# Optimization experiments

Hardware: AMD Instinct MI355X
Metric: run time of the kernel (lower is better)

## Reference

```python
import jax, jax.numpy as jnp
import numpy as np

N, M, D = 16384, 1024, 32


def setup_inputs() -> dict:
    key = jax.random.key(0)
    k1, k2 = jax.random.split(key)
    x = jax.random.normal(k1, (N, D), dtype=jnp.float32)
    centers = jax.random.normal(k2, (M, D), dtype=jnp.float32)
    sigma = jnp.ones((M, D), dtype=jnp.float32)  # get_sigma_ones(s=1.0)
    return {"x": x, "centers": centers, "sigma": sigma}


def reference(x, centers, sigma):
    # Gaussian RBF kernel: exp(-0.5 * delta^T invCov delta) / sqrt((2pi)^D det(S))
    d = x.shape[1]
    s2 = sigma ** 2  # (M, D)
    # invCovMat: inverse of per-center diagonal covariance -> diag(1/s2)
    invCov = jnp.eye(d, dtype=x.dtype) * (1.0 / s2)[:, :, None]  # (M, D, D)
    # denom: sqrt((2pi)^D * prod(s2))
    k = (2.0 * np.pi) ** d  # python float, safe for D=32 in f32
    detS = jnp.sqrt(jnp.asarray(k, x.dtype) * jnp.prod(s2, axis=1))  # (M,)
    delta = x[:, None, :] - centers[None, :, :]  # (N, M, D)
    # batched (1,D) @ (D,D) per (n,m) pair, then elementwise * delta and reduce
    q = jnp.einsum('nmd,mde->nme', delta, invCov)  # (N, M, D)
    X = jnp.sum(q * delta, axis=2)  # (N, M) squared Mahalanobis distance
    return jnp.exp(-0.5 * X) / detS[None, :]  # (N, M)
```

## Files before the change

kernel.cpp:

```cpp
#include <hip/hip_runtime.h>


#define N_  16384
#define M_  1024
#define D_  32
#define NT  32
#define BLK 256

typedef float v2f __attribute__((ext_vector_type(2)));

__global__ __launch_bounds__(BLK) void rbf_kernel(
    const float* __restrict__ x, const float* __restrict__ centers,
    const float* __restrict__ sigma, float* __restrict__ out)
{
    const int tid = threadIdx.x;
    const int m   = blockIdx.x * BLK + tid;
    const int n0  = blockIdx.y * NT;

    __shared__ float r2s[NT];

    if (tid < NT) {
        const float4* xr = (const float4*)(x + (size_t)(n0 + tid) * D_);
        float a0 = 0.f, a1 = 0.f, a2 = 0.f, a3 = 0.f;
        #pragma unroll
        for (int k = 0; k < D_ / 4; ++k) {
            float4 v = xr[k];
            a0 = fmaf(v.x, v.x, a0); a1 = fmaf(v.y, v.y, a1);
            a2 = fmaf(v.z, v.z, a2); a3 = fmaf(v.w, v.w, a3);
        }
        r2s[tid] = (a0 + a1) + (a2 + a3);
    }
    __syncthreads();

    const float L2E      = 1.4426950408889634f;
    const float LOG2_2PI = 2.6514961294723187f;

    float s2_0 = 0.f, ld = 0.f;
    bool uf = true;
    {
        const float* sg = sigma + (size_t)m * D_;
        #pragma unroll
        for (int d = 0; d < D_; ++d) {
            float s  = sg[d];
            float s2 = s * s;
            if (d == 0) s2_0 = s2;
            uf = uf && (s2 == s2_0);
            ld += log2f(s2);
        }
    }

    if (__all((int)uf)) {
        const float w0 = 1.0f / s2_0;
        v2f av[D_ / 2];
        float b = 0.f;
        {
            const v2f* cg = (const v2f*)(centers + (size_t)m * D_);
            #pragma unroll
            for (int j = 0; j < D_ / 2; ++j) {
                v2f c = cg[j];
                v2f a = c * w0;
                av[j] = a;
                b = fmaf(c.x, a.x, b);
                b = fmaf(c.y, a.y, b);
            }
        }
        const float c0 = fmaf(-0.5f * L2E, b, -0.5f * (D_ * LOG2_2PI + ld));
        const float qc = -0.5f * L2E * w0;

        float* o0 = out + (size_t)n0 * M_ + m;
        #pragma unroll 1
        for (int i = 0; i < NT; i += 2) {
            const v2f* xr0 = (const v2f*)(x + (size_t)(n0 + i) * D_);
            const v2f* xr1 = xr0 + (D_ / 2);
            v2f p0 = {0.f,0.f}, p1 = {0.f,0.f};
            v2f q0 = {0.f,0.f}, q1 = {0.f,0.f};
            #pragma unroll
            for (int j = 0; j < D_ / 2; j += 2) {
                p0 += xr0[j]     * av[j];
                p1 += xr0[j + 1] * av[j + 1];
                q0 += xr1[j]     * av[j];
                q1 += xr1[j + 1] * av[j + 1];
            }
            v2f ps = p0 + p1;
            v2f qs = q0 + q1;
            float f0 = fmaf(L2E, ps.x + ps.y, fmaf(qc, r2s[i],     c0));
            float f1 = fmaf(L2E, qs.x + qs.y, fmaf(qc, r2s[i + 1], c0));
            __builtin_nontemporal_store(__builtin_amdgcn_exp2f(f0), o0 + (size_t)i * M_);
            __builtin_nontemporal_store(__builtin_amdgcn_exp2f(f1), o0 + (size_t)(i + 1) * M_);
        }
    } else {
        const float c0 = -0.5f * (D_ * LOG2_2PI + ld);
        const float* cg = centers + (size_t)m * D_;
        const float* sg = sigma   + (size_t)m * D_;
        #pragma unroll 1
        for (int i = 0; i < NT; ++i) {
            const float* xr = x + (size_t)(n0 + i) * D_;
            float a0 = 0.f, a1 = 0.f;
            #pragma unroll
            for (int d = 0; d < D_; d += 2) {
                float s0 = sg[d], s1 = sg[d + 1];
                float t0 = xr[d]     - cg[d];
                float t1 = xr[d + 1] - cg[d + 1];
                a0 = fmaf(t0 * (1.0f / (s0 * s0)), t0, a0);
                a1 = fmaf(t1 * (1.0f / (s1 * s1)), t1, a1);
            }
            float f = fmaf(-0.5f * L2E, a0 + a1, c0);
            out[(size_t)(n0 + i) * M_ + m] = __builtin_amdgcn_exp2f(f);
        }
    }
}

extern "C" void kernel_launch(void* const* d_in, const int* in_sizes, int n_in,
                              void* d_out, int out_size, void* d_ws, size_t ws_size,
                              hipStream_t stream) {
    const float* x = (const float*)d_in[0];
    const float* c = (const float*)d_in[1];
    const float* s = (const float*)d_in[2];
    float* out = (float*)d_out;
    dim3 grid(M_ / BLK, N_ / NT);
    rbf_kernel<<<grid, BLK, 0, stream>>>(x, c, s, out);
}
```

Measured before the change: 97.66 us.

## Stage x tile and center/sigma rows in LDS, two centers per thread

After: 94.66 us. -3.1%, faster.

```diff
diff --git a/kernel.cpp b/kernel.cpp
--- a/kernel.cpp
+++ b/kernel.cpp
@@ -1,111 +1,160 @@
 #include <hip/hip_runtime.h>
 
 
-#define N_  16384
-#define M_  1024
-#define D_  32
-#define NT  32
-#define BLK 256
+#define N_   16384
+#define M_   1024
+#define D_   32
+#define NT   64
+#define BLK  256
+#define MW   (BLK / 64)
+#define SSTR 33
 
-typedef float v2f __attribute__((ext_vector_type(2)));
+typedef float v4f __attribute__((ext_vector_type(4)));
 
-__global__ __launch_bounds__(BLK) void rbf_kernel(
+__global__ __launch_bounds__(BLK, 2) void rbf_kernel(
     const float* __restrict__ x, const float* __restrict__ centers,
     const float* __restrict__ sigma, float* __restrict__ out)
 {
-    const int tid = threadIdx.x;
-    const int m   = blockIdx.x * BLK + tid;
-    const int n0  = blockIdx.y * NT;
+    const int tid  = threadIdx.x;
+    const int lane = tid & 63;
+    const int wv   = tid >> 6;
+    const int n0   = blockIdx.y * NT;
+    const int mbA  = blockIdx.x * (BLK * 2) + wv * 64;
+    const int mbB  = mbA + BLK;
 
+    __shared__ float xs[NT * D_];
     __shared__ float r2s[NT];
+    __shared__ float scr[MW][64 * SSTR];
 
-    if (tid < NT) {
-        const float4* xr = (const float4*)(x + (size_t)(n0 + tid) * D_);
-        float a0 = 0.f, a1 = 0.f, a2 = 0.f, a3 = 0.f;
+    {
+        const float4* xg  = (const float4*)(x + (size_t)n0 * D_);
+        float4*       xs4 = (float4*)xs;
         #pragma unroll
-        for (int k = 0; k < D_ / 4; ++k) {
-            float4 v = xr[k];
-            a0 = fmaf(v.x, v.x, a0); a1 = fmaf(v.y, v.y, a1);
-            a2 = fmaf(v.z, v.z, a2); a3 = fmaf(v.w, v.w, a3);
+        for (int j = 0; j < (NT * D_ / 4) / BLK; ++j) {
+            int f = j * BLK + tid;
+            float4 v = xg[f];
+            xs4[f] = v;
+            float s = fmaf(v.x, v.x, fmaf(v.y, v.y, fmaf(v.z, v.z, v.w * v.w)));
+            s += __shfl_xor(s, 1);
+            s += __shfl_xor(s, 2);
+            s += __shfl_xor(s, 4);
+            if ((tid & 7) == 0) r2s[f >> 3] = s;
         }
-        r2s[tid] = (a0 + a1) + (a2 + a3);
     }
     __syncthreads();
+
+    float* sw = scr[wv];
+
+    auto stagechunk = [&](const float* P, int mbase) {
+        const float4* P4 = (const float4*)(P + (size_t)mbase * D_);
+        #pragma unroll
+        for (int k = 0; k < 8; ++k) {
+            int f = k * 64 + lane;
+            float4 v = P4[f];
+            int off = (f >> 3) * SSTR + (f & 7) * 4;
+            sw[off + 0] = v.x; sw[off + 1] = v.y;
+            sw[off + 2] = v.z; sw[off + 3] = v.w;
+        }
+    };
+
+    auto sigscan = [&](int mbase, float& s2_0, float& ld) -> bool {
+        stagechunk(sigma, mbase);
+        const float* row = sw + lane * SSTR;
+        float s0 = row[0];
+        s2_0 = s0 * s0;
+        bool uf = true; ld = 0.f;
+        #pragma unroll
+        for (int d = 0; d < D_; ++d) {
+            float s  = row[d];
+            float s2 = s * s;
+            uf = uf && (s2 == s2_0);
+            ld += log2f(s2);
+        }
+        return uf;
+    };
+
+    auto cscan = [&](int mbase, float w0, v4f* A) -> float {
+        stagechunk(centers, mbase);
+        const float* row = sw + lane * SSTR;
+        float b = 0.f;
+        #pragma unroll
+        for (int k = 0; k < 8; ++k) {
+            v4f c = { row[4*k], row[4*k+1], row[4*k+2], row[4*k+3] };
+            v4f a = c * w0;
+            A[k] = a;
+            b = fmaf(c.x, a.x, fmaf(c.y, a.y, fmaf(c.z, a.z, fmaf(c.w, a.w, b))));
+        }
+        return b;
+    };
+
+    float s2A, ldA, s2B, ldB;
+    v4f A0[8], A1[8];
+    bool ufA = sigscan(mbA, s2A, ldA);
+    const float w0A = 1.0f / s2A;
+    float bA = cscan(mbA, w0A, A0);
+    bool ufB = sigscan(mbB, s2B, ldB);
+    const float w0B = 1.0f / s2B;
+    float bB = cscan(mbB, w0B, A1);
 
     const float L2E      = 1.4426950408889634f;
     const float LOG2_2PI = 2.6514961294723187f;
 
-    float s2_0 = 0.f, ld = 0.f;
-    bool uf = true;
-    {
-        const float* sg = sigma + (size_t)m * D_;
+    if (__all((int)(ufA && ufB))) {
         #pragma unroll
-        for (int d = 0; d < D_; ++d) {
-            float s  = sg[d];
-            float s2 = s * s;
-            if (d == 0) s2_0 = s2;
-            uf = uf && (s2 == s2_0);
-            ld += log2f(s2);
+        for (int k = 0; k < 8; ++k) {
+            asm volatile("" : "+v"(A0[k]));
+            asm volatile("" : "+v"(A1[k]));
         }
-    }
+        const float c0A = fmaf(-0.5f * L2E, bA, -0.5f * (D_ * LOG2_2PI + ldA));
+        const float c0B = fmaf(-0.5f * L2E, bB, -0.5f * (D_ * LOG2_2PI + ldB));
+        const float qcA = -0.5f * L2E * w0A;
+        const float qcB = -0.5f * L2E * w0B;
 
-    if (__all((int)uf)) {
-        const float w0 = 1.0f / s2_0;
-        v2f av[D_ / 2];
-        float b = 0.f;
-        {
-            const v2f* cg = (const v2f*)(centers + (size_t)m * D_);
+        float* oA = out + (size_t)n0 * M_ + mbA + lane;
+        float* oB = oA + BLK;
+        #pragma unroll 1
+        for (int i = 0; i < NT; ++i) {
+            const v4f* xr = (const v4f*)(xs + i * D_);
+            v4f pa = {0,0,0,0}, pb = {0,0,0,0};
+            v4f qa = {0,0,0,0}, qb = {0,0,0,0};
             #pragma unroll
-            for (int j = 0; j < D_ / 2; ++j) {
-                v2f c = cg[j];
-                v2f a = c * w0;
-                av[j] = a;
-                b = fmaf(c.x, a.x, b);
-                b = fmaf(c.y, a.y, b);
+            for (int k = 0; k < 8; k += 2) {
+                v4f x0 = xr[k], x1 = xr[k + 1];
+                pa += x0 * A0[k];     pb += x1 * A0[k + 1];
+                qa += x0 * A1[k];     qb += x1 * A1[k + 1];
             }
-        }
-        const float c0 = fmaf(-0.5f * L2E, b, -0.5f * (D_ * LOG2_2PI + ld));
-        const float qc = -0.5f * L2E * w0;
-
-        float* o0 = out + (size_t)n0 * M_ + m;
-        #pragma unroll 1
-        for (int i = 0; i < NT; i += 2) {
-            const v2f* xr0 = (const v2f*)(x + (size_t)(n0 + i) * D_);
-            const v2f* xr1 = xr0 + (D_ / 2);
-            v2f p0 = {0.f,0.f}, p1 = {0.f,0.f};
-            v2f q0 = {0.f,0.f}, q1 = {0.f,0.f};
-            #pragma unroll
-            for (int j = 0; j < D_ / 2; j += 2) {
-                p0 += xr0[j]     * av[j];
-                p1 += xr0[j + 1] * av[j + 1];
-                q0 += xr1[j]     * av[j];
-                q1 += xr1[j + 1] * av[j + 1];
-            }
-            v2f ps = p0 + p1;
-            v2f qs = q0 + q1;
-            float f0 = fmaf(L2E, ps.x + ps.y, fmaf(qc, r2s[i],     c0));
-            float f1 = fmaf(L2E, qs.x + qs.y, fmaf(qc, r2s[i + 1], c0));
-            __builtin_nontemporal_store(__builtin_amdgcn_exp2f(f0), o0 + (size_t)i * M_);
-            __builtin_nontemporal_store(__builtin_amdgcn_exp2f(f1), o0 + (size_t)(i + 1) * M_);
+            v4f ps = pa + pb, qs = qa + qb;
+            float SA = (ps.x + ps.y) + (ps.z + ps.w);
+            float SB = (qs.x + qs.y) + (qs.z + qs.w);
+            float r2 = r2s[i];
+            float fA = fmaf(L2E, SA, fmaf(qcA, r2, c0A));
+            float fB = fmaf(L2E, SB, fmaf(qcB, r2, c0B));
+            __builtin_nontemporal_store(__builtin_amdgcn_exp2f(fA), oA + (size_t)i * M_);
+            __builtin_nontemporal_store(__builtin_amdgcn_exp2f(fB), oB + (size_t)i * M_);
         }
     } else {
-        const float c0 = -0.5f * (D_ * LOG2_2PI + ld);
-        const float* cg = centers + (size_t)m * D_;
-        const float* sg = sigma   + (size_t)m * D_;
         #pragma unroll 1
-        for (int i = 0; i < NT; ++i) {
-            const float* xr = x + (size_t)(n0 + i) * D_;
-            float a0 = 0.f, a1 = 0.f;
-            #pragma unroll
-            for (int d = 0; d < D_; d += 2) {
-                float s0 = sg[d], s1 = sg[d + 1];
-                float t0 = xr[d]     - cg[d];
-                float t1 = xr[d + 1] - cg[d + 1];
-                a0 = fmaf(t0 * (1.0f / (s0 * s0)), t0, a0);
-                a1 = fmaf(t1 * (1.0f / (s1 * s1)), t1, a1);
+        for (int half = 0; half < 2; ++half) {
+            const int m = (half ? mbB : mbA) + lane;
+            const float* cg = centers + (size_t)m * D_;
+            const float* sg = sigma   + (size_t)m * D_;
+            const float ld  = half ? ldB : ldA;
+            const float c0  = -0.5f * (D_ * LOG2_2PI + ld);
+            #pragma unroll 1
+            for (int i = 0; i < NT; ++i) {
+                const float* xr = xs + i * D_;
+                float a0 = 0.f, a1 = 0.f;
+                #pragma unroll
+                for (int d = 0; d < D_; d += 2) {
+                    float s0 = sg[d], s1 = sg[d + 1];
+                    float t0 = xr[d]     - cg[d];
+                    float t1 = xr[d + 1] - cg[d + 1];
+                    a0 = fmaf(t0 * (1.0f / (s0 * s0)), t0, a0);
+                    a1 = fmaf(t1 * (1.0f / (s1 * s1)), t1, a1);
+                }
+                float f = fmaf(-0.5f * L2E, a0 + a1, c0);
+                out[(size_t)(n0 + i) * M_ + m] = __builtin_amdgcn_exp2f(f);
             }
-            float f = fmaf(-0.5f * L2E, a0 + a1, c0);
-            out[(size_t)(n0 + i) * M_ + m] = __builtin_amdgcn_exp2f(f);
         }
     }
 }
@@ -117,6 +166,6 @@
     const float* c = (const float*)d_in[1];
     const float* s = (const float*)d_in[2];
     float* out = (float*)d_out;
-    dim3 grid(M_ / BLK, N_ / NT);
+    dim3 grid(M_ / (BLK * 2), N_ / NT);
     rbf_kernel<<<grid, BLK, 0, stream>>>(x, c, s, out);
 }
```

## Register-block four centers per thread and stage x tile in LDS

Applied to the files above, without the earlier changes.

After: 113.0 us. 15.7% more time.

```diff
diff --git a/kernel.cpp b/kernel.cpp
--- a/kernel.cpp
+++ b/kernel.cpp
@@ -1,111 +1,136 @@
 #include <hip/hip_runtime.h>
 
 
-#define N_  16384
-#define M_  1024
-#define D_  32
-#define NT  32
-#define BLK 256
+#define N_   16384
+#define M_   1024
+#define D_   32
+#define NT   16
+#define BLK  256
 
 typedef float v2f __attribute__((ext_vector_type(2)));
+typedef float v4f __attribute__((ext_vector_type(4)));
 
-__global__ __launch_bounds__(BLK) void rbf_kernel(
+__global__ __launch_bounds__(BLK, 3) void rbf_kernel(
     const float* __restrict__ x, const float* __restrict__ centers,
     const float* __restrict__ sigma, float* __restrict__ out)
 {
     const int tid = threadIdx.x;
-    const int m   = blockIdx.x * BLK + tid;
-    const int n0  = blockIdx.y * NT;
+    const int n0  = blockIdx.x * NT;
+    const int m0  = tid * 4;
 
+    __shared__ float xs[NT * D_];
     __shared__ float r2s[NT];
 
-    if (tid < NT) {
-        const float4* xr = (const float4*)(x + (size_t)(n0 + tid) * D_);
-        float a0 = 0.f, a1 = 0.f, a2 = 0.f, a3 = 0.f;
-        #pragma unroll
-        for (int k = 0; k < D_ / 4; ++k) {
-            float4 v = xr[k];
-            a0 = fmaf(v.x, v.x, a0); a1 = fmaf(v.y, v.y, a1);
-            a2 = fmaf(v.z, v.z, a2); a3 = fmaf(v.w, v.w, a3);
-        }
-        r2s[tid] = (a0 + a1) + (a2 + a3);
+    if (tid < NT * D_ / 4) {
+        const float4* xg = (const float4*)(x + (size_t)n0 * D_);
+        float4 v = xg[tid];
+        ((float4*)xs)[tid] = v;
+        float s = fmaf(v.x, v.x, fmaf(v.y, v.y, fmaf(v.z, v.z, v.w * v.w)));
+        s += __shfl_xor(s, 1);
+        s += __shfl_xor(s, 2);
+        s += __shfl_xor(s, 4);
+        if ((tid & 7) == 0) r2s[tid >> 3] = s;
     }
     __syncthreads();
 
     const float L2E      = 1.4426950408889634f;
     const float LOG2_2PI = 2.6514961294723187f;
 
-    float s2_0 = 0.f, ld = 0.f;
+    float s2h[4], ldh[4];
     bool uf = true;
     {
-        const float* sg = sigma + (size_t)m * D_;
+        const float* sg = sigma + (size_t)m0 * D_;
         #pragma unroll
-        for (int d = 0; d < D_; ++d) {
-            float s  = sg[d];
-            float s2 = s * s;
-            if (d == 0) s2_0 = s2;
-            uf = uf && (s2 == s2_0);
-            ld += log2f(s2);
+        for (int h = 0; h < 4; ++h) {
+            float ld = 0.f, s20 = 0.f;
+            bool u = true;
+            #pragma unroll
+            for (int d = 0; d < D_; ++d) {
+                float s  = sg[h * D_ + d];
+                float s2 = s * s;
+                if (d == 0) s20 = s2;
+                u = u && (s2 == s20);
+                ld += log2f(s2);
+            }
+            s2h[h] = s20; ldh[h] = ld;
+            uf = uf && u;
         }
     }
 
     if (__all((int)uf)) {
-        const float w0 = 1.0f / s2_0;
-        v2f av[D_ / 2];
-        float b = 0.f;
+        v4f  A[4][8];
+        float c0[4], qc[4];
         {
-            const v2f* cg = (const v2f*)(centers + (size_t)m * D_);
+            const v4f* cg = (const v4f*)(centers + (size_t)m0 * D_);
             #pragma unroll
-            for (int j = 0; j < D_ / 2; ++j) {
-                v2f c = cg[j];
-                v2f a = c * w0;
-                av[j] = a;
-                b = fmaf(c.x, a.x, b);
-                b = fmaf(c.y, a.y, b);
+            for (int h = 0; h < 4; ++h) {
+                float w0 = 1.0f / s2h[h];
+                float b  = 0.f;
+                #pragma unroll
+                for (int k = 0; k < 8; ++k) {
+                    v4f c = cg[h * 8 + k];
+                    v4f a = c * w0;
+                    A[h][k] = a;
+                    b = fmaf(c.x, a.x, fmaf(c.y, a.y, fmaf(c.z, a.z, fmaf(c.w, a.w, b))));
+                }
+                c0[h] = fmaf(-0.5f * L2E, b, -0.5f * (D_ * LOG2_2PI + ldh[h]));
+                qc[h] = -0.5f * L2E * w0;
             }
         }
-        const float c0 = fmaf(-0.5f * L2E, b, -0.5f * (D_ * LOG2_2PI + ld));
-        const float qc = -0.5f * L2E * w0;
+        #pragma unroll
+        for (int h = 0; h < 4; ++h)
+            #pragma unroll
+            for (int k = 0; k < 8; ++k)
+                asm volatile("" : "+v"(A[h][k]));
 
-        float* o0 = out + (size_t)n0 * M_ + m;
+        v4f* o = (v4f*)(out + (size_t)n0 * M_ + m0);
         #pragma unroll 1
-        for (int i = 0; i < NT; i += 2) {
-            const v2f* xr0 = (const v2f*)(x + (size_t)(n0 + i) * D_);
-            const v2f* xr1 = xr0 + (D_ / 2);
-            v2f p0 = {0.f,0.f}, p1 = {0.f,0.f};
-            v2f q0 = {0.f,0.f}, q1 = {0.f,0.f};
+        for (int i = 0; i < NT; ++i) {
+            const v4f* xr = (const v4f*)(xs + i * D_);
+            v2f a0 = {0,0}, a1 = {0,0}, a2 = {0,0}, a3 = {0,0};
             #pragma unroll
-            for (int j = 0; j < D_ / 2; j += 2) {
-                p0 += xr0[j]     * av[j];
-                p1 += xr0[j + 1] * av[j + 1];
-                q0 += xr1[j]     * av[j];
-                q1 += xr1[j + 1] * av[j + 1];
+            for (int k = 0; k < 8; ++k) {
+                v4f xv  = xr[k];
+                v2f xlo = {xv.x, xv.y}, xhi = {xv.z, xv.w};
+                v2f l0 = {A[0][k].x, A[0][k].y}, h0 = {A[0][k].z, A[0][k].w};
+                v2f l1 = {A[1][k].x, A[1][k].y}, h1 = {A[1][k].z, A[1][k].w};
+                v2f l2 = {A[2][k].x, A[2][k].y}, h2 = {A[2][k].z, A[2][k].w};
+                v2f l3 = {A[3][k].x, A[3][k].y}, h3 = {A[3][k].z, A[3][k].w};
+                a0 += xlo * l0; a0 += xhi * h0;
+                a1 += xlo * l1; a1 += xhi * h1;
+                a2 += xlo * l2; a2 += xhi * h2;
+                a3 += xlo * l3; a3 += xhi * h3;
             }
-            v2f ps = p0 + p1;
-            v2f qs = q0 + q1;
-            float f0 = fmaf(L2E, ps.x + ps.y, fmaf(qc, r2s[i],     c0));
-            float f1 = fmaf(L2E, qs.x + qs.y, fmaf(qc, r2s[i + 1], c0));
-            __builtin_nontemporal_store(__builtin_amdgcn_exp2f(f0), o0 + (size_t)i * M_);
-            __builtin_nontemporal_store(__builtin_amdgcn_exp2f(f1), o0 + (size_t)(i + 1) * M_);
+            float r2 = r2s[i];
+            v4f e;
+            e.x = __builtin_amdgcn_exp2f(fmaf(L2E, a0.x + a0.y, fmaf(qc[0], r2, c0[0])));
+            e.y = __builtin_amdgcn_exp2f(fmaf(L2E, a1.x + a1.y, fmaf(qc[1], r2, c0[1])));
+            e.z = __builtin_amdgcn_exp2f(fmaf(L2E, a2.x + a2.y, fmaf(qc[2], r2, c0[2])));
+            e.w = __builtin_amdgcn_exp2f(fmaf(L2E, a3.x + a3.y, fmaf(qc[3], r2, c0[3])));
+            o[i * (M_ / 4)] = e;
         }
     } else {
-        const float c0 = -0.5f * (D_ * LOG2_2PI + ld);
-        const float* cg = centers + (size_t)m * D_;
-        const float* sg = sigma   + (size_t)m * D_;
         #pragma unroll 1
-        for (int i = 0; i < NT; ++i) {
-            const float* xr = x + (size_t)(n0 + i) * D_;
-            float a0 = 0.f, a1 = 0.f;
-            #pragma unroll
-            for (int d = 0; d < D_; d += 2) {
-                float s0 = sg[d], s1 = sg[d + 1];
-                float t0 = xr[d]     - cg[d];
-                float t1 = xr[d + 1] - cg[d + 1];
-                a0 = fmaf(t0 * (1.0f / (s0 * s0)), t0, a0);
-                a1 = fmaf(t1 * (1.0f / (s1 * s1)), t1, a1);
+        for (int h = 0; h < 4; ++h) {
+            const int m = m0 + h;
+            const float* cg = centers + (size_t)m * D_;
+            const float* sg = sigma   + (size_t)m * D_;
+            const float c0 = -0.5f * (D_ * LOG2_2PI + ldh[h]);
+            #pragma unroll 1
+            for (int i = 0; i < NT; ++i) {
+                const float* xr = xs + i * D_;
+                float b0 = 0.f, b1 = 0.f;
+                #pragma unroll
+                for (int d = 0; d < D_; d += 2) {
+                    float s0 = sg[d], s1 = sg[d + 1];
+                    float t0 = xr[d]     - cg[d];
+                    float t1 = xr[d + 1] - cg[d + 1];
+                    b0 = fmaf(t0 * (1.0f / (s0 * s0)), t0, b0);
+                    b1 = fmaf(t1 * (1.0f / (s1 * s1)), t1, b1);
+                }
+                float f = fmaf(-0.5f * L2E, b0 + b1, c0);
+                out[(size_t)(n0 + i) * M_ + m] = __builtin_amdgcn_exp2f(f);
             }
-            float f = fmaf(-0.5f * L2E, a0 + a1, c0);
-            out[(size_t)(n0 + i) * M_ + m] = __builtin_amdgcn_exp2f(f);
         }
     }
 }
@@ -117,6 +142,5 @@
     const float* c = (const float*)d_in[1];
     const float* s = (const float*)d_in[2];
     float* out = (float*)d_out;
-    dim3 grid(M_ / BLK, N_ / NT);
-    rbf_kernel<<<grid, BLK, 0, stream>>>(x, c, s, out);
+    rbf_kernel<<<dim3(N_ / NT), BLK, 0, stream>>>(x, c, s, out);
 }
```
